# Performance work log

Measured on AMD Instinct MI355X. Metric: run time of the kernel, lower is better.

## Reference

```python
import jax, jax.numpy as jnp
import numpy as np

N, T, D, H = 256, 128, 512, 1024

def setup_inputs() -> dict:
    key = jax.random.key(0)
    k = jax.random.split(key, 5)
    x = jax.random.normal(k[0], (N, T, D), dtype=jnp.float32)
    A = jax.random.normal(k[1], (N, H, 4, 4), dtype=jnp.float32)
    Wx = jax.random.normal(k[2], (D, 4 * H), dtype=jnp.float32) / np.sqrt(D)
    Wh = jax.random.normal(k[3], (H, 4 * H), dtype=jnp.float32) / np.sqrt(H)
    Wattn = jax.random.normal(k[4], (H, 4 * H), dtype=jnp.float32) / np.sqrt(H)
    b = jnp.zeros((4 * H,), dtype=jnp.float32)
    return {"x": x, "A": A, "Wx": Wx, "Wh": Wh, "Wattn": Wattn, "b": b}

def reference(x, A, Wx, Wh, Wattn, b):
    n, h_dim = A.shape[0], A.shape[1]
    A_flat = A.reshape(n, h_dim, -1)            # (N, H, L), L = 16 spatial locations
    h0 = A_flat.mean(axis=-1)                   # avg-pooled image feature
    c0 = h0
    scale = 1.0 / jnp.sqrt(jnp.asarray(h_dim, dtype=x.dtype))

    def step(carry, x_t):
        h, c = carry
        # scaled dot-product attention over the 4x4 feature grid
        scores = jnp.einsum('nhl,nh->nl', A_flat, h) * scale
        w = jax.nn.softmax(scores, axis=1)
        attn = jnp.einsum('nhl,nl->nh', A_flat, w)
        gates = x_t @ Wx + h @ Wh + attn @ Wattn + b  # (N, 4H)
        i, f, o, g = jnp.split(gates, 4, axis=1)
        c_next = jax.nn.sigmoid(f) * c + jax.nn.sigmoid(i) * jnp.tanh(g)
        h_next = jax.nn.sigmoid(o) * jnp.tanh(c_next)
        return (h_next, c_next), h_next

    (_, _), hs = jax.lax.scan(step, (h0, c0), jnp.swapaxes(x, 0, 1))
    return jnp.swapaxes(hs, 0, 1)               # (N, T, H)
```

## Files before the change

kernel.cpp:

```cpp
#include <hip/hip_runtime.h>

#define Nn 256
#define Tt 128
#define Dd 512
#define Hh 1024
#define G4 4096
#define KK 2560
#define KSTEP 1536
#define KHALF 768

typedef __attribute__((ext_vector_type(8))) short s8v;
typedef __attribute__((ext_vector_type(4))) short s4v;
typedef __attribute__((ext_vector_type(4))) float f4v;

__device__ __forceinline__ float bf2f(ushort u) {
    union { unsigned int i; float f; } v; v.i = ((unsigned int)u) << 16; return v.f;
}
__device__ __forceinline__ ushort f2bf(float f) {
    union { float f; unsigned int i; } v; v.f = f;
    unsigned int x = v.i;
    return (ushort)((x + 0x7fffu + ((x >> 16) & 1u)) >> 16);
}
__device__ __forceinline__ void split2(float f, ushort& hi, ushort& lo) {
    hi = f2bf(f);
    lo = f2bf(f - bf2f(hi));
}

__global__ __launch_bounds__(256) void prep_W(
    const float* __restrict__ Wx, const float* __restrict__ Wh,
    const float* __restrict__ Wa, ushort* __restrict__ Whi,
    ushort* __restrict__ Wlo)
{
    __shared__ float tile[64 * 65];
    int kb = blockIdx.x * 64;
    int jb = blockIdx.y * 64;
    const float* src; int kofs;
    if (kb < Dd)            { src = Wx; kofs = kb; }
    else if (kb < Dd + Hh)  { src = Wh; kofs = kb - Dd; }
    else                    { src = Wa; kofs = kb - Dd - Hh; }
    int tid = threadIdx.x;
    int r = tid >> 2;
    int c16 = (tid & 3) * 16;
    const float* sp = src + (size_t)(kofs + r) * G4 + jb + c16;
    #pragma unroll
    for (int i = 0; i < 16; i++) tile[(c16 + i) * 65 + r] = sp[i];
    __syncthreads();
    ushort hi[16], lo[16];
    #pragma unroll
    for (int i = 0; i < 16; i++) split2(tile[r * 65 + c16 + i], hi[i], lo[i]);
    size_t o = (size_t)(jb + r) * KK + kb + c16;
    #pragma unroll
    for (int p = 0; p < 2; p++) {
        s8v vh, vl;
        #pragma unroll
        for (int i = 0; i < 8; i++) { vh[i] = (short)hi[p * 8 + i]; vl[i] = (short)lo[p * 8 + i]; }
        *(s8v*)&Whi[o + p * 8] = vh;
        *(s8v*)&Wlo[o + p * 8] = vl;
    }
}

__global__ __launch_bounds__(256) void prep_A(
    const float* __restrict__ A, ushort* __restrict__ Athi,
    ushort* __restrict__ Atlo)
{
    int n = blockIdx.x;
    int tid = threadIdx.x;
    int h0 = tid * 4;
    float v[4][16];
    #pragma unroll
    for (int r = 0; r < 4; r++) {
        const f4v* p = (const f4v*)(A + ((size_t)n * Hh + h0 + r) * 16);
        #pragma unroll
        for (int q = 0; q < 4; q++) {
            f4v xv = p[q];
            v[r][q * 4 + 0] = xv[0]; v[r][q * 4 + 1] = xv[1];
            v[r][q * 4 + 2] = xv[2]; v[r][q * 4 + 3] = xv[3];
        }
    }
    #pragma unroll
    for (int l = 0; l < 16; l++) {
        s4v vh, vl;
        #pragma unroll
        for (int r = 0; r < 4; r++) {
            ushort hi, lo; split2(v[r][l], hi, lo);
            vh[r] = (short)hi; vl[r] = (short)lo;
        }
        size_t o = ((size_t)n * 16 + l) * Hh + h0;
        *(s4v*)&Athi[o] = vh;
        *(s4v*)&Atlo[o] = vl;
    }
}

__global__ __launch_bounds__(256) void aw_gemm(
    const ushort* __restrict__ Athi, const ushort* __restrict__ Atlo,
    const ushort* __restrict__ Whi, const ushort* __restrict__ Wlo,
    float* __restrict__ AW)
{
    __shared__ ushort Ahi[64 * 72], Alo[64 * 72];
    __shared__ ushort Bhi[64 * 72], Blo[64 * 72];
    int j0 = blockIdx.x * 64;
    int m0 = blockIdx.y * 64;
    int tid = threadIdx.x;
    int lane = tid & 63, wave = tid >> 6;
    int l15 = lane & 15, quad = lane >> 4;
    f4v acc[4];
    #pragma unroll
    for (int s = 0; s < 4; s++) acc[s] = (f4v){0.f, 0.f, 0.f, 0.f};
    int rs = tid >> 3;
    int cs = (tid & 7) * 8;
    for (int kb = 0; kb < Hh; kb += 64) {
        __syncthreads();
        #pragma unroll
        for (int p = 0; p < 2; p++) {
            int r = rs + 32 * p;
            size_t oa = (size_t)(m0 + r) * Hh + kb + cs;
            *(s8v*)&Ahi[r * 72 + cs] = *(const s8v*)&Athi[oa];
            *(s8v*)&Alo[r * 72 + cs] = *(const s8v*)&Atlo[oa];
            size_t ob = (size_t)(j0 + r) * KK + (Dd + Hh) + kb + cs;
            *(s8v*)&Bhi[r * 72 + cs] = *(const s8v*)&Whi[ob];
            *(s8v*)&Blo[r * 72 + cs] = *(const s8v*)&Wlo[ob];
        }
        __syncthreads();
        #pragma unroll
        for (int ks = 0; ks < 2; ks++) {
            s8v ah = *(const s8v*)&Ahi[(wave * 16 + l15) * 72 + ks * 32 + quad * 8];
            s8v al = *(const s8v*)&Alo[(wave * 16 + l15) * 72 + ks * 32 + quad * 8];
            #pragma unroll
            for (int s = 0; s < 4; s++) {
                s8v bh = *(const s8v*)&Bhi[(s * 16 + l15) * 72 + ks * 32 + quad * 8];
                s8v bl = *(const s8v*)&Blo[(s * 16 + l15) * 72 + ks * 32 + quad * 8];
                acc[s] = __builtin_amdgcn_mfma_f32_16x16x32_bf16(ah, bh, acc[s], 0, 0, 0);
                acc[s] = __builtin_amdgcn_mfma_f32_16x16x32_bf16(ah, bl, acc[s], 0, 0, 0);
                acc[s] = __builtin_amdgcn_mfma_f32_16x16x32_bf16(al, bh, acc[s], 0, 0, 0);
            }
        }
    }
    #pragma unroll
    for (int s = 0; s < 4; s++) {
        int j = j0 + s * 16 + l15;
        #pragma unroll
        for (int rr = 0; rr < 4; rr++) {
            int row = m0 + wave * 16 + quad * 4 + rr;
            AW[(size_t)row * G4 + j] = acc[s][rr];
        }
    }
}

__global__ __launch_bounds__(256) void init_h0(
    const float* __restrict__ A, float* __restrict__ h, float* __restrict__ c,
    ushort* __restrict__ hhi, ushort* __restrict__ hlo)
{
    int i = blockIdx.x * 256 + threadIdx.x;
    const float* ap = A + (size_t)i * 16;
    float s = 0.f;
    #pragma unroll
    for (int l = 0; l < 16; l++) s += ap[l];
    s *= (1.f / 16.f);
    h[i] = s; c[i] = s;
    ushort hi, lo; split2(s, hi, lo);
    hhi[i] = hi; hlo[i] = lo;
}

__global__ __launch_bounds__(256) void calc_w(
    const float* __restrict__ A, const float* __restrict__ h,
    float* __restrict__ wbuf)
{
    int n = blockIdx.x;
    int tid = threadIdx.x;
    int lane = tid & 63, wave = tid >> 6;
    __shared__ float red[4][16];
    float part[16];
    #pragma unroll
    for (int l = 0; l < 16; l++) part[l] = 0.f;
    #pragma unroll
    for (int rr = 0; rr < 4; rr++) {
        int hh = tid + rr * 256;
        float hv = h[n * Hh + hh];
        const f4v* ap = (const f4v*)(A + ((size_t)n * Hh + hh) * 16);
        #pragma unroll
        for (int q = 0; q < 4; q++) {
            f4v v = ap[q];
            part[q * 4 + 0] += v[0] * hv; part[q * 4 + 1] += v[1] * hv;
            part[q * 4 + 2] += v[2] * hv; part[q * 4 + 3] += v[3] * hv;
        }
    }
    #pragma unroll
    for (int l = 0; l < 16; l++) {
        float v = part[l];
        #pragma unroll
        for (int off = 32; off > 0; off >>= 1) v += __shfl_down(v, off);
        if (lane == 0) red[wave][l] = v;
    }
    __syncthreads();
    if (tid == 0) {
        float sc[16]; float mx = -3.4e38f;
        #pragma unroll
        for (int l = 0; l < 16; l++) {
            sc[l] = (red[0][l] + red[1][l] + red[2][l] + red[3][l]) * 0.03125f;
            mx = fmaxf(mx, sc[l]);
        }
        float sum = 0.f;
        #pragma unroll
        for (int l = 0; l < 16; l++) { sc[l] = expf(sc[l] - mx); sum += sc[l]; }
        float inv = 1.f / sum;
        #pragma unroll
        for (int l = 0; l < 16; l++) wbuf[n * 16 + l] = sc[l] * inv;
    }
}

__global__ __launch_bounds__(256) void gemm_half(
    const float* __restrict__ x,
    const ushort* __restrict__ hhi, const ushort* __restrict__ hlo,
    const ushort* __restrict__ Whi, const ushort* __restrict__ Wlo,
    float* __restrict__ g0, float* __restrict__ g1, int t)
{
    __shared__ ushort Ahi[64 * 72], Alo[64 * 72];
    __shared__ ushort Bhi[64 * 72], Blo[64 * 72];
    int j0 = blockIdx.x * 64;
    int n0 = blockIdx.y * 64;
    int kb0 = blockIdx.z * KHALF;
    float* gout = blockIdx.z ? g1 : g0;
    int tid = threadIdx.x;
    int lane = tid & 63, wave = tid >> 6;
    int l15 = lane & 15, quad = lane >> 4;
    f4v acc[4];
    #pragma unroll
    for (int s = 0; s < 4; s++) acc[s] = (f4v){0.f, 0.f, 0.f, 0.f};

    int rs = tid >> 3;
    int cs = (tid & 7) * 8;

    for (int kb = kb0; kb < kb0 + KHALF; kb += 64) {
        __syncthreads();
        if (kb < Dd) {
            const float* xs = x + (size_t)t * Dd + kb + cs;
            #pragma unroll
            for (int p = 0; p < 2; p++) {
                int r = rs + 32 * p;
                const float* ap = xs + (size_t)(n0 + r) * (Tt * Dd);
                s8v vh, vl;
                #pragma unroll
                for (int i = 0; i < 8; i++) {
                    ushort hi_, lo_; split2(ap[i], hi_, lo_);
                    vh[i] = (short)hi_; vl[i] = (short)lo_;
                }
                *(s8v*)&Ahi[r * 72 + cs] = vh;
                *(s8v*)&Alo[r * 72 + cs] = vl;
            }
        } else {
            int kofs = kb - Dd;
            #pragma unroll
            for (int p = 0; p < 2; p++) {
                int r = rs + 32 * p;
                size_t o = (size_t)(n0 + r) * Hh + kofs + cs;
                *(s8v*)&Ahi[r * 72 + cs] = *(const s8v*)&hhi[o];
                *(s8v*)&Alo[r * 72 + cs] = *(const s8v*)&hlo[o];
            }
        }
        #pragma unroll
        for (int p = 0; p < 2; p++) {
            int r = rs + 32 * p;
            size_t o = (size_t)(j0 + r) * KK + kb + cs;
            *(s8v*)&Bhi[r * 72 + cs] = *(const s8v*)&Whi[o];
            *(s8v*)&Blo[r * 72 + cs] = *(const s8v*)&Wlo[o];
        }
        __syncthreads();
        #pragma unroll
        for (int ks = 0; ks < 2; ks++) {
            s8v ah = *(const s8v*)&Ahi[(wave * 16 + l15) * 72 + ks * 32 + quad * 8];
            s8v al = *(const s8v*)&Alo[(wave * 16 + l15) * 72 + ks * 32 + quad * 8];
            #pragma unroll
            for (int s = 0; s < 4; s++) {
                s8v bh = *(const s8v*)&Bhi[(s * 16 + l15) * 72 + ks * 32 + quad * 8];
                s8v bl = *(const s8v*)&Blo[(s * 16 + l15) * 72 + ks * 32 + quad * 8];
                acc[s] = __builtin_amdgcn_mfma_f32_16x16x32_bf16(ah, bh, acc[s], 0, 0, 0);
                acc[s] = __builtin_amdgcn_mfma_f32_16x16x32_bf16(ah, bl, acc[s], 0, 0, 0);
                acc[s] = __builtin_amdgcn_mfma_f32_16x16x32_bf16(al, bh, acc[s], 0, 0, 0);
            }
        }
    }
    #pragma unroll
    for (int s = 0; s < 4; s++) {
        int j = j0 + s * 16 + l15;
        #pragma unroll
        for (int rr = 0; rr < 4; rr++) {
            int row = n0 + wave * 16 + quad * 4 + rr;
            gout[(size_t)row * G4 + j] = acc[s][rr];
        }
    }
}

__global__ __launch_bounds__(256) void lstm_fused(
    const float* __restrict__ g0, const float* __restrict__ g1,
    const float* __restrict__ bias, const float* __restrict__ AW,
    float* __restrict__ wbuf, const float* __restrict__ A,
    float* __restrict__ c, ushort* __restrict__ hhi, ushort* __restrict__ hlo,
    float* __restrict__ out, int t)
{
    int n = blockIdx.x;
    int tid = threadIdx.x;
    int lane = tid & 63, wave = tid >> 6;
    int j4 = tid * 4;
    __shared__ float wsh[16];
    __shared__ float red[4][16];
    if (tid < 16) wsh[tid] = wbuf[n * 16 + tid];
    __syncthreads();
    float w[16];
    #pragma unroll
    for (int l = 0; l < 16; l++) w[l] = wsh[l];

    f4v acc[4];
    #pragma unroll
    for (int q = 0; q < 4; q++) acc[q] = (f4v){0.f, 0.f, 0.f, 0.f};
    const float* awp = AW + (size_t)n * 16 * G4;
    #pragma unroll
    for (int l = 0; l < 16; l++) {
        float wl = w[l];
        #pragma unroll
        for (int q = 0; q < 4; q++) {
            f4v v = *(const f4v*)&awp[(size_t)l * G4 + q * Hh + j4];
            acc[q][0] += wl * v[0]; acc[q][1] += wl * v[1];
            acc[q][2] += wl * v[2]; acc[q][3] += wl * v[3];
        }
    }

    size_t base = (size_t)n * G4;
    f4v gv[4];
    #pragma unroll
    for (int q = 0; q < 4; q++) {
        f4v a0 = *(const f4v*)&g0[base + q * Hh + j4];
        f4v a1 = *(const f4v*)&g1[base + q * Hh + j4];
        f4v bv = *(const f4v*)&bias[q * Hh + j4];
        #pragma unroll
        for (int e = 0; e < 4; e++) gv[q][e] = a0[e] + a1[e] + bv[e] + acc[q][e];
    }
    int i4 = n * Hh + j4;
    f4v cold = *(const f4v*)&c[i4];
    f4v cnew, hnew;
    #pragma unroll
    for (int e = 0; e < 4; e++) {
        float si = 1.f / (1.f + expf(-gv[0][e]));
        float sf = 1.f / (1.f + expf(-gv[1][e]));
        float so = 1.f / (1.f + expf(-gv[2][e]));
        float tg = tanhf(gv[3][e]);
        float cn = sf * cold[e] + si * tg;
        float hn = so * tanhf(cn);
        cnew[e] = cn; hnew[e] = hn;
    }
    *(f4v*)&c[i4] = cnew;
    s4v vh, vl;
    #pragma unroll
    for (int e = 0; e < 4; e++) {
        ushort hi, lo; split2(hnew[e], hi, lo);
        vh[e] = (short)hi; vl[e] = (short)lo;
    }
    *(s4v*)&hhi[i4] = vh;
    *(s4v*)&hlo[i4] = vl;
    *(f4v*)&out[((size_t)n * Tt + t) * Hh + j4] = hnew;

    float part[16];
    #pragma unroll
    for (int l = 0; l < 16; l++) part[l] = 0.f;
    #pragma unroll
    for (int r = 0; r < 4; r++) {
        float hv = hnew[r];
        const f4v* ap = (const f4v*)(A + ((size_t)n * Hh + j4 + r) * 16);
        #pragma unroll
        for (int q = 0; q < 4; q++) {
            f4v v = ap[q];
            part[q * 4 + 0] += v[0] * hv; part[q * 4 + 1] += v[1] * hv;
            part[q * 4 + 2] += v[2] * hv; part[q * 4 + 3] += v[3] * hv;
        }
    }
    #pragma unroll
    for (int l = 0; l < 16; l++) {
        float v = part[l];
        #pragma unroll
        for (int off = 32; off > 0; off >>= 1) v += __shfl_down(v, off);
        if (lane == 0) red[wave][l] = v;
    }
    __syncthreads();
    if (tid == 0) {
        float sc[16]; float mx = -3.4e38f;
        #pragma unroll
        for (int l = 0; l < 16; l++) {
            sc[l] = (red[0][l] + red[1][l] + red[2][l] + red[3][l]) * 0.03125f;
            mx = fmaxf(mx, sc[l]);
        }
        float sum = 0.f;
        #pragma unroll
        for (int l = 0; l < 16; l++) { sc[l] = expf(sc[l] - mx); sum += sc[l]; }
        float inv = 1.f / sum;
        #pragma unroll
        for (int l = 0; l < 16; l++) wbuf[n * 16 + l] = sc[l] * inv;
    }
}

extern "C" void kernel_launch(void* const* d_in, const int* in_sizes, int n_in,
                              void* d_out, int out_size, void* d_ws, size_t ws_size,
                              hipStream_t stream)
{
    const float* x  = (const float*)d_in[0];
    const float* A  = (const float*)d_in[1];
    const float* Wx = (const float*)d_in[2];
    const float* Wh = (const float*)d_in[3];
    const float* Wa = (const float*)d_in[4];
    const float* b  = (const float*)d_in[5];
    float* out = (float*)d_out;

    char* p = (char*)d_ws;
    ushort* Whi  = (ushort*)p;  p += (size_t)G4 * KK * 2;
    ushort* Wlo  = (ushort*)p;  p += (size_t)G4 * KK * 2;
    float*  h    = (float*)p;   p += (size_t)Nn * Hh * 4;
    float*  c    = (float*)p;   p += (size_t)Nn * Hh * 4;
    float*  g0   = (float*)p;   p += (size_t)Nn * G4 * 4;
    float*  g1   = (float*)p;   p += (size_t)Nn * G4 * 4;
    ushort* hhi  = (ushort*)p;  p += (size_t)Nn * Hh * 2;
    ushort* hlo  = (ushort*)p;  p += (size_t)Nn * Hh * 2;
    ushort* Athi = (ushort*)p;  p += (size_t)Nn * 16 * Hh * 2;
    ushort* Atlo = (ushort*)p;  p += (size_t)Nn * 16 * Hh * 2;
    float*  AW   = (float*)p;   p += (size_t)Nn * 16 * G4 * 4;
    float*  wbuf = (float*)p;   p += (size_t)Nn * 16 * 4;

    prep_W<<<dim3(KK / 64, G4 / 64), 256, 0, stream>>>(Wx, Wh, Wa, Whi, Wlo);
    prep_A<<<Nn, 256, 0, stream>>>(A, Athi, Atlo);
    aw_gemm<<<dim3(G4 / 64, (Nn * 16) / 64), 256, 0, stream>>>(
        Athi, Atlo, Whi, Wlo, AW);
    init_h0<<<(Nn * Hh) / 256, 256, 0, stream>>>(A, h, c, hhi, hlo);
    calc_w<<<Nn, 256, 0, stream>>>(A, h, wbuf);
    for (int t = 0; t < Tt; t++) {
        gemm_half<<<dim3(G4 / 64, Nn / 64, 2), 256, 0, stream>>>(
            x, hhi, hlo, Whi, Wlo, g0, g1, t);
        lstm_fused<<<Nn, 256, 0, stream>>>(
            g0, g1, b, AW, wbuf, A, c, hhi, hlo, out, t);
    }
}
```

Baseline: 5.936 ms.

## Double-buffer per-step GEMM with register prefetch and 128-row tiles

Rewrites the per-timestep gate GEMM to use two LDS buffers. The next K-slice of global data is loaded into registers while MFMAs run on the current slice, which leaves one barrier per iteration instead of two. The tile grows from 64 to 128 rows of N so each wave computes two 16-row subtiles, reusing B fragments and halving the number of weight loads per output. It also vectorizes the fp32 x loads. In exchange, the grid shrinks from 512 to 256 blocks, and LDS and register use rise, which limits occupancy (launch_bounds 256,1).

```diff
diff --git a/kernel.cpp b/kernel.cpp
--- a/kernel.cpp
+++ b/kernel.cpp
@@ -8,6 +8,7 @@
 #define KK 2560
 #define KSTEP 1536
 #define KHALF 768
+#define NIT 12
 
 typedef __attribute__((ext_vector_type(8))) short s8v;
 typedef __attribute__((ext_vector_type(4))) short s4v;
@@ -208,84 +209,126 @@
     }
 }
 
-__global__ __launch_bounds__(256) void gemm_half(
+__global__ __launch_bounds__(256, 1) void gemm_step(
     const float* __restrict__ x,
     const ushort* __restrict__ hhi, const ushort* __restrict__ hlo,
     const ushort* __restrict__ Whi, const ushort* __restrict__ Wlo,
     float* __restrict__ g0, float* __restrict__ g1, int t)
 {
-    __shared__ ushort Ahi[64 * 72], Alo[64 * 72];
-    __shared__ ushort Bhi[64 * 72], Blo[64 * 72];
-    int j0 = blockIdx.x * 64;
-    int n0 = blockIdx.y * 64;
-    int kb0 = blockIdx.z * KHALF;
+    __shared__ ushort Ah[2][128 * 72], Al[2][128 * 72];
+    __shared__ ushort Bh[2][64 * 72],  Bl[2][64 * 72];
+    const int j0 = blockIdx.x * 64;
+    const int n0 = blockIdx.y * 128;
+    const int kb0 = blockIdx.z * KHALF;
     float* gout = blockIdx.z ? g1 : g0;
-    int tid = threadIdx.x;
-    int lane = tid & 63, wave = tid >> 6;
-    int l15 = lane & 15, quad = lane >> 4;
-    f4v acc[4];
-    #pragma unroll
-    for (int s = 0; s < 4; s++) acc[s] = (f4v){0.f, 0.f, 0.f, 0.f};
-
-    int rs = tid >> 3;
-    int cs = (tid & 7) * 8;
-
-    for (int kb = kb0; kb < kb0 + KHALF; kb += 64) {
-        __syncthreads();
-        if (kb < Dd) {
-            const float* xs = x + (size_t)t * Dd + kb + cs;
-            #pragma unroll
-            for (int p = 0; p < 2; p++) {
-                int r = rs + 32 * p;
-                const float* ap = xs + (size_t)(n0 + r) * (Tt * Dd);
+    const int tid = threadIdx.x;
+    const int lane = tid & 63, wave = tid >> 6;
+    const int l15 = lane & 15, quad = lane >> 4;
+    const int rs = tid >> 3, cs = (tid & 7) * 8;
+
+    f4v acc[2][4];
+    #pragma unroll
+    for (int rt = 0; rt < 2; rt++)
+        #pragma unroll
+        for (int ct = 0; ct < 4; ct++) acc[rt][ct] = (f4v){0.f, 0.f, 0.f, 0.f};
+
+    f4v xr[4][2];
+    s8v arh[4], arl[4];
+    s8v brh[2], brl[2];
+    int ldx = 0;
+
+    auto LOADT = [&](int kb) {
+        ldx = (kb < Dd) ? 1 : 0;
+        if (ldx) {
+            #pragma unroll
+            for (int p = 0; p < 4; p++) {
+                const f4v* ap = (const f4v*)(x + ((size_t)(n0 + rs + 32 * p) * Tt + t) * Dd + kb + cs);
+                xr[p][0] = ap[0]; xr[p][1] = ap[1];
+            }
+        } else {
+            int ko = kb - Dd;
+            #pragma unroll
+            for (int p = 0; p < 4; p++) {
+                size_t o = (size_t)(n0 + rs + 32 * p) * Hh + ko + cs;
+                arh[p] = *(const s8v*)&hhi[o];
+                arl[p] = *(const s8v*)&hlo[o];
+            }
+        }
+        #pragma unroll
+        for (int p = 0; p < 2; p++) {
+            size_t o = (size_t)(j0 + rs + 32 * p) * KK + kb + cs;
+            brh[p] = *(const s8v*)&Whi[o];
+            brl[p] = *(const s8v*)&Wlo[o];
+        }
+    };
+    auto WRITET = [&](int b) {
+        if (ldx) {
+            #pragma unroll
+            for (int p = 0; p < 4; p++) {
                 s8v vh, vl;
                 #pragma unroll
-                for (int i = 0; i < 8; i++) {
-                    ushort hi_, lo_; split2(ap[i], hi_, lo_);
+                for (int i = 0; i < 4; i++) {
+                    ushort hi_, lo_;
+                    split2(xr[p][0][i], hi_, lo_);
                     vh[i] = (short)hi_; vl[i] = (short)lo_;
+                    split2(xr[p][1][i], hi_, lo_);
+                    vh[i + 4] = (short)hi_; vl[i + 4] = (short)lo_;
                 }
-                *(s8v*)&Ahi[r * 72 + cs] = vh;
-                *(s8v*)&Alo[r * 72 + cs] = vl;
+                *(s8v*)&Ah[b][(rs + 32 * p) * 72 + cs] = vh;
+                *(s8v*)&Al[b][(rs + 32 * p) * 72 + cs] = vl;
             }
         } else {
-            int kofs = kb - Dd;
-            #pragma unroll
-            for (int p = 0; p < 2; p++) {
-                int r = rs + 32 * p;
-                size_t o = (size_t)(n0 + r) * Hh + kofs + cs;
-                *(s8v*)&Ahi[r * 72 + cs] = *(const s8v*)&hhi[o];
-                *(s8v*)&Alo[r * 72 + cs] = *(const s8v*)&hlo[o];
+            #pragma unroll
+            for (int p = 0; p < 4; p++) {
+                *(s8v*)&Ah[b][(rs + 32 * p) * 72 + cs] = arh[p];
+                *(s8v*)&Al[b][(rs + 32 * p) * 72 + cs] = arl[p];
             }
         }
         #pragma unroll
         for (int p = 0; p < 2; p++) {
-            int r = rs + 32 * p;
-            size_t o = (size_t)(j0 + r) * KK + kb + cs;
-            *(s8v*)&Bhi[r * 72 + cs] = *(const s8v*)&Whi[o];
-            *(s8v*)&Blo[r * 72 + cs] = *(const s8v*)&Wlo[o];
-        }
+            *(s8v*)&Bh[b][(rs + 32 * p) * 72 + cs] = brh[p];
+            *(s8v*)&Bl[b][(rs + 32 * p) * 72 + cs] = brl[p];
+        }
+    };
+
+    LOADT(kb0);
+    WRITET(0);
+    __syncthreads();
+    int cur = 0;
+    for (int it = 0; it < NIT; it++) {
+        if (it + 1 < NIT) LOADT(kb0 + (it + 1) * 64);
+        #pragma unroll
+        for (int ks = 0; ks < 2; ks++) {
+            s8v ah0 = *(const s8v*)&Ah[cur][(wave * 32 + l15) * 72 + ks * 32 + quad * 8];
+            s8v ah1 = *(const s8v*)&Ah[cur][(wave * 32 + 16 + l15) * 72 + ks * 32 + quad * 8];
+            s8v al0 = *(const s8v*)&Al[cur][(wave * 32 + l15) * 72 + ks * 32 + quad * 8];
+            s8v al1 = *(const s8v*)&Al[cur][(wave * 32 + 16 + l15) * 72 + ks * 32 + quad * 8];
+            #pragma unroll
+            for (int ct = 0; ct < 4; ct++) {
+                s8v bh = *(const s8v*)&Bh[cur][(ct * 16 + l15) * 72 + ks * 32 + quad * 8];
+                s8v bl = *(const s8v*)&Bl[cur][(ct * 16 + l15) * 72 + ks * 32 + quad * 8];
+                acc[0][ct] = __builtin_amdgcn_mfma_f32_16x16x32_bf16(ah0, bh, acc[0][ct], 0, 0, 0);
+                acc[0][ct] = __builtin_amdgcn_mfma_f32_16x16x32_bf16(ah0, bl, acc[0][ct], 0, 0, 0);
+                acc[0][ct] = __builtin_amdgcn_mfma_f32_16x16x32_bf16(al0, bh, acc[0][ct], 0, 0, 0);
+                acc[1][ct] = __builtin_amdgcn_mfma_f32_16x16x32_bf16(ah1, bh, acc[1][ct], 0, 0, 0);
+                acc[1][ct] = __builtin_amdgcn_mfma_f32_16x16x32_bf16(ah1, bl, acc[1][ct], 0, 0, 0);
+                acc[1][ct] = __builtin_amdgcn_mfma_f32_16x16x32_bf16(al1, bh, acc[1][ct], 0, 0, 0);
+            }
+        }
+        if (it + 1 < NIT) WRITET(cur ^ 1);
         __syncthreads();
-        #pragma unroll
-        for (int ks = 0; ks < 2; ks++) {
-            s8v ah = *(const s8v*)&Ahi[(wave * 16 + l15) * 72 + ks * 32 + quad * 8];
-            s8v al = *(const s8v*)&Alo[(wave * 16 + l15) * 72 + ks * 32 + quad * 8];
-            #pragma unroll
-            for (int s = 0; s < 4; s++) {
-                s8v bh = *(const s8v*)&Bhi[(s * 16 + l15) * 72 + ks * 32 + quad * 8];
-                s8v bl = *(const s8v*)&Blo[(s * 16 + l15) * 72 + ks * 32 + quad * 8];
-                acc[s] = __builtin_amdgcn_mfma_f32_16x16x32_bf16(ah, bh, acc[s], 0, 0, 0);
-                acc[s] = __builtin_amdgcn_mfma_f32_16x16x32_bf16(ah, bl, acc[s], 0, 0, 0);
-                acc[s] = __builtin_amdgcn_mfma_f32_16x16x32_bf16(al, bh, acc[s], 0, 0, 0);
-            }
-        }
-    }
-    #pragma unroll
-    for (int s = 0; s < 4; s++) {
-        int j = j0 + s * 16 + l15;
-        #pragma unroll
-        for (int rr = 0; rr < 4; rr++) {
-            int row = n0 + wave * 16 + quad * 4 + rr;
-            gout[(size_t)row * G4 + j] = acc[s][rr];
+        cur ^= 1;
+    }
+    #pragma unroll
+    for (int rt = 0; rt < 2; rt++) {
+        #pragma unroll
+        for (int ct = 0; ct < 4; ct++) {
+            int j = j0 + ct * 16 + l15;
+            #pragma unroll
+            for (int rr = 0; rr < 4; rr++) {
+                int row = n0 + wave * 32 + rt * 16 + quad * 4 + rr;
+                gout[(size_t)row * G4 + j] = acc[rt][ct][rr];
+            }
         }
     }
 }
@@ -429,7 +472,7 @@
     init_h0<<<(Nn * Hh) / 256, 256, 0, stream>>>(A, h, c, hhi, hlo);
     calc_w<<<Nn, 256, 0, stream>>>(A, h, wbuf);
     for (int t = 0; t < Tt; t++) {
-        gemm_half<<<dim3(G4 / 64, Nn / 64, 2), 256, 0, stream>>>(
+        gemm_step<<<dim3(G4 / 64, Nn / 128, 2), 256, 0, stream>>>(
             x, hhi, hlo, Whi, Wlo, g0, g1, t);
         lstm_fused<<<Nn, 256, 0, stream>>>(
             g0, g1, b, AW, wbuf, A, c, hhi, hlo, out, t);
```

Result: no change. 6.023 ms (+1.5%).

## Use 128-row tiles with four-way split-K in step GEMM, store AW as fp16

Applied to the files above, without the earlier changes.

The per-step gate GEMM now uses 128x64 output tiles, with each wave computing two 16-row subtiles, and splits K into four 384-wide slices instead of two 768-wide ones. This keeps the grid at 512 blocks while reusing each loaded W tile across twice as many batch rows, which cuts W traffic per step. The precomputed attention projection AW is stored in fp16 instead of fp32, halving the bytes lstm_fused reads from it every step. In exchange, lstm_fused must read four partial-sum buffers instead of two, and the fp16 AW adds rounding error.

```diff
diff --git a/kernel.cpp b/kernel.cpp
--- a/kernel.cpp
+++ b/kernel.cpp
@@ -7,11 +7,14 @@
 #define G4 4096
 #define KK 2560
 #define KSTEP 1536
-#define KHALF 768
+#define KQ 384
+#define NIT 6
 
 typedef __attribute__((ext_vector_type(8))) short s8v;
 typedef __attribute__((ext_vector_type(4))) short s4v;
 typedef __attribute__((ext_vector_type(4))) float f4v;
+typedef _Float16 f16;
+typedef __attribute__((ext_vector_type(4))) _Float16 h4v;
 
 __device__ __forceinline__ float bf2f(ushort u) {
     union { unsigned int i; float f; } v; v.i = ((unsigned int)u) << 16; return v.f;
@@ -94,7 +97,7 @@
 __global__ __launch_bounds__(256) void aw_gemm(
     const ushort* __restrict__ Athi, const ushort* __restrict__ Atlo,
     const ushort* __restrict__ Whi, const ushort* __restrict__ Wlo,
-    float* __restrict__ AW)
+    f16* __restrict__ AW)
 {
     __shared__ ushort Ahi[64 * 72], Alo[64 * 72];
     __shared__ ushort Bhi[64 * 72], Blo[64 * 72];
@@ -141,7 +144,7 @@
         #pragma unroll
         for (int rr = 0; rr < 4; rr++) {
             int row = m0 + wave * 16 + quad * 4 + rr;
-            AW[(size_t)row * G4 + j] = acc[s][rr];
+            AW[(size_t)row * G4 + j] = (f16)acc[s][rr];
         }
     }
 }
@@ -208,34 +211,38 @@
     }
 }
 
-__global__ __launch_bounds__(256) void gemm_half(
+__global__ __launch_bounds__(256) void gemm_step(
     const float* __restrict__ x,
     const ushort* __restrict__ hhi, const ushort* __restrict__ hlo,
     const ushort* __restrict__ Whi, const ushort* __restrict__ Wlo,
-    float* __restrict__ g0, float* __restrict__ g1, int t)
-{
-    __shared__ ushort Ahi[64 * 72], Alo[64 * 72];
-    __shared__ ushort Bhi[64 * 72], Blo[64 * 72];
-    int j0 = blockIdx.x * 64;
-    int n0 = blockIdx.y * 64;
-    int kb0 = blockIdx.z * KHALF;
-    float* gout = blockIdx.z ? g1 : g0;
-    int tid = threadIdx.x;
-    int lane = tid & 63, wave = tid >> 6;
-    int l15 = lane & 15, quad = lane >> 4;
-    f4v acc[4];
-    #pragma unroll
-    for (int s = 0; s < 4; s++) acc[s] = (f4v){0.f, 0.f, 0.f, 0.f};
-
-    int rs = tid >> 3;
-    int cs = (tid & 7) * 8;
-
-    for (int kb = kb0; kb < kb0 + KHALF; kb += 64) {
+    float* __restrict__ g0, float* __restrict__ g1,
+    float* __restrict__ g2, float* __restrict__ g3, int t)
+{
+    __shared__ ushort Ah[128 * 72], Al[128 * 72];
+    __shared__ ushort Bh[64 * 72],  Bl[64 * 72];
+    const int j0 = blockIdx.x * 64;
+    const int n0 = blockIdx.y * 128;
+    const int kz = blockIdx.z;
+    const int kb0 = kz * KQ;
+    float* gout = (kz == 0) ? g0 : (kz == 1) ? g1 : (kz == 2) ? g2 : g3;
+    const int tid = threadIdx.x;
+    const int lane = tid & 63, wave = tid >> 6;
+    const int l15 = lane & 15, quad = lane >> 4;
+    const int rs = tid >> 3, cs = (tid & 7) * 8;
+
+    f4v acc[2][4];
+    #pragma unroll
+    for (int rt = 0; rt < 2; rt++)
+        #pragma unroll
+        for (int ct = 0; ct < 4; ct++) acc[rt][ct] = (f4v){0.f, 0.f, 0.f, 0.f};
+
+    for (int it = 0; it < NIT; it++) {
+        int kb = kb0 + it * 64;
         __syncthreads();
         if (kb < Dd) {
             const float* xs = x + (size_t)t * Dd + kb + cs;
             #pragma unroll
-            for (int p = 0; p < 2; p++) {
+            for (int p = 0; p < 4; p++) {
                 int r = rs + 32 * p;
                 const float* ap = xs + (size_t)(n0 + r) * (Tt * Dd);
                 s8v vh, vl;
@@ -244,55 +251,64 @@
                     ushort hi_, lo_; split2(ap[i], hi_, lo_);
                     vh[i] = (short)hi_; vl[i] = (short)lo_;
                 }
-                *(s8v*)&Ahi[r * 72 + cs] = vh;
-                *(s8v*)&Alo[r * 72 + cs] = vl;
+                *(s8v*)&Ah[r * 72 + cs] = vh;
+                *(s8v*)&Al[r * 72 + cs] = vl;
             }
         } else {
-            int kofs = kb - Dd;
+            int ko = kb - Dd;
             #pragma unroll
-            for (int p = 0; p < 2; p++) {
+            for (int p = 0; p < 4; p++) {
                 int r = rs + 32 * p;
-                size_t o = (size_t)(n0 + r) * Hh + kofs + cs;
-                *(s8v*)&Ahi[r * 72 + cs] = *(const s8v*)&hhi[o];
-                *(s8v*)&Alo[r * 72 + cs] = *(const s8v*)&hlo[o];
+                size_t o = (size_t)(n0 + r) * Hh + ko + cs;
+                *(s8v*)&Ah[r * 72 + cs] = *(const s8v*)&hhi[o];
+                *(s8v*)&Al[r * 72 + cs] = *(const s8v*)&hlo[o];
             }
         }
         #pragma unroll
         for (int p = 0; p < 2; p++) {
             int r = rs + 32 * p;
             size_t o = (size_t)(j0 + r) * KK + kb + cs;
-            *(s8v*)&Bhi[r * 72 + cs] = *(const s8v*)&Whi[o];
-            *(s8v*)&Blo[r * 72 + cs] = *(const s8v*)&Wlo[o];
+            *(s8v*)&Bh[r * 72 + cs] = *(const s8v*)&Whi[o];
+            *(s8v*)&Bl[r * 72 + cs] = *(const s8v*)&Wlo[o];
         }
         __syncthreads();
         #pragma unroll
         for (int ks = 0; ks < 2; ks++) {
-            s8v ah = *(const s8v*)&Ahi[(wave * 16 + l15) * 72 + ks * 32 + quad * 8];
-            s8v al = *(const s8v*)&Alo[(wave * 16 + l15) * 72 + ks * 32 + quad * 8];
+            s8v ah0 = *(const s8v*)&Ah[(wave * 32 + l15) * 72 + ks * 32 + quad * 8];
+            s8v ah1 = *(const s8v*)&Ah[(wave * 32 + 16 + l15) * 72 + ks * 32 + quad * 8];
+            s8v al0 = *(const s8v*)&Al[(wave * 32 + l15) * 72 + ks * 32 + quad * 8];
+            s8v al1 = *(const s8v*)&Al[(wave * 32 + 16 + l15) * 72 + ks * 32 + quad * 8];
             #pragma unroll
-            for (int s = 0; s < 4; s++) {
-                s8v bh = *(const s8v*)&Bhi[(s * 16 + l15) * 72 + ks * 32 + quad * 8];
-                s8v bl = *(const s8v*)&Blo[(s * 16 + l15) * 72 + ks * 32 + quad * 8];
-                acc[s] = __builtin_amdgcn_mfma_f32_16x16x32_bf16(ah, bh, acc[s], 0, 0, 0);
-                acc[s] = __builtin_amdgcn_mfma_f32_16x16x32_bf16(ah, bl, acc[s], 0, 0, 0);
-                acc[s] = __builtin_amdgcn_mfma_f32_16x16x32_bf16(al, bh, acc[s], 0, 0, 0);
+            for (int ct = 0; ct < 4; ct++) {
+                s8v bh = *(const s8v*)&Bh[(ct * 16 + l15) * 72 + ks * 32 + quad * 8];
+                s8v bl = *(const s8v*)&Bl[(ct * 16 + l15) * 72 + ks * 32 + quad * 8];
+                acc[0][ct] = __builtin_amdgcn_mfma_f32_16x16x32_bf16(ah0, bh, acc[0][ct], 0, 0, 0);
+                acc[0][ct] = __builtin_amdgcn_mfma_f32_16x16x32_bf16(ah0, bl, acc[0][ct], 0, 0, 0);
+                acc[0][ct] = __builtin_amdgcn_mfma_f32_16x16x32_bf16(al0, bh, acc[0][ct], 0, 0, 0);
+                acc[1][ct] = __builtin_amdgcn_mfma_f32_16x16x32_bf16(ah1, bh, acc[1][ct], 0, 0, 0);
+                acc[1][ct] = __builtin_amdgcn_mfma_f32_16x16x32_bf16(ah1, bl, acc[1][ct], 0, 0, 0);
+                acc[1][ct] = __builtin_amdgcn_mfma_f32_16x16x32_bf16(al1, bh, acc[1][ct], 0, 0, 0);
             }
         }
     }
     #pragma unroll
-    for (int s = 0; s < 4; s++) {
-        int j = j0 + s * 16 + l15;
-        #pragma unroll
-        for (int rr = 0; rr < 4; rr++) {
-            int row = n0 + wave * 16 + quad * 4 + rr;
-            gout[(size_t)row * G4 + j] = acc[s][rr];
+    for (int rt = 0; rt < 2; rt++) {
+        #pragma unroll
+        for (int ct = 0; ct < 4; ct++) {
+            int j = j0 + ct * 16 + l15;
+            #pragma unroll
+            for (int rr = 0; rr < 4; rr++) {
+                int row = n0 + wave * 32 + rt * 16 + quad * 4 + rr;
+                gout[(size_t)row * G4 + j] = acc[rt][ct][rr];
+            }
         }
     }
 }
 
 __global__ __launch_bounds__(256) void lstm_fused(
     const float* __restrict__ g0, const float* __restrict__ g1,
-    const float* __restrict__ bias, const float* __restrict__ AW,
+    const float* __restrict__ g2, const float* __restrict__ g3,
+    const float* __restrict__ bias, const f16* __restrict__ AW,
     float* __restrict__ wbuf, const float* __restrict__ A,
     float* __restrict__ c, ushort* __restrict__ hhi, ushort* __restrict__ hlo,
     float* __restrict__ out, int t)
@@ -312,15 +328,15 @@
     f4v acc[4];
     #pragma unroll
     for (int q = 0; q < 4; q++) acc[q] = (f4v){0.f, 0.f, 0.f, 0.f};
-    const float* awp = AW + (size_t)n * 16 * G4;
+    const f16* awp = AW + (size_t)n * 16 * G4;
     #pragma unroll
     for (int l = 0; l < 16; l++) {
         float wl = w[l];
         #pragma unroll
         for (int q = 0; q < 4; q++) {
-            f4v v = *(const f4v*)&awp[(size_t)l * G4 + q * Hh + j4];
-            acc[q][0] += wl * v[0]; acc[q][1] += wl * v[1];
-            acc[q][2] += wl * v[2]; acc[q][3] += wl * v[3];
+            h4v v = *(const h4v*)&awp[(size_t)l * G4 + q * Hh + j4];
+            acc[q][0] += wl * (float)v[0]; acc[q][1] += wl * (float)v[1];
+            acc[q][2] += wl * (float)v[2]; acc[q][3] += wl * (float)v[3];
         }
     }
 
@@ -330,9 +346,12 @@
     for (int q = 0; q < 4; q++) {
         f4v a0 = *(const f4v*)&g0[base + q * Hh + j4];
         f4v a1 = *(const f4v*)&g1[base + q * Hh + j4];
+        f4v a2 = *(const f4v*)&g2[base + q * Hh + j4];
+        f4v a3 = *(const f4v*)&g3[base + q * Hh + j4];
         f4v bv = *(const f4v*)&bias[q * Hh + j4];
         #pragma unroll
-        for (int e = 0; e < 4; e++) gv[q][e] = a0[e] + a1[e] + bv[e] + acc[q][e];
+        for (int e = 0; e < 4; e++)
+            gv[q][e] = (a0[e] + a1[e]) + (a2[e] + a3[e]) + bv[e] + acc[q][e];
     }
     int i4 = n * Hh + j4;
     f4v cold = *(const f4v*)&c[i4];
@@ -415,11 +434,13 @@
     float*  c    = (float*)p;   p += (size_t)Nn * Hh * 4;
     float*  g0   = (float*)p;   p += (size_t)Nn * G4 * 4;
     float*  g1   = (float*)p;   p += (size_t)Nn * G4 * 4;
+    float*  g2   = (float*)p;   p += (size_t)Nn * G4 * 4;
+    float*  g3   = (float*)p;   p += (size_t)Nn * G4 * 4;
     ushort* hhi  = (ushort*)p;  p += (size_t)Nn * Hh * 2;
     ushort* hlo  = (ushort*)p;  p += (size_t)Nn * Hh * 2;
     ushort* Athi = (ushort*)p;  p += (size_t)Nn * 16 * Hh * 2;
     ushort* Atlo = (ushort*)p;  p += (size_t)Nn * 16 * Hh * 2;
-    float*  AW   = (float*)p;   p += (size_t)Nn * 16 * G4 * 4;
+    f16*    AW   = (f16*)p;     p += (size_t)Nn * 16 * G4 * 2;
     float*  wbuf = (float*)p;   p += (size_t)Nn * 16 * 4;
 
     prep_W<<<dim3(KK / 64, G4 / 64), 256, 0, stream>>>(Wx, Wh, Wa, Whi, Wlo);
@@ -429,9 +450,9 @@
     init_h0<<<(Nn * Hh) / 256, 256, 0, stream>>>(A, h, c, hhi, hlo);
     calc_w<<<Nn, 256, 0, stream>>>(A, h, wbuf);
     for (int t = 0; t < Tt; t++) {
-        gemm_half<<<dim3(G4 / 64, Nn / 64, 2), 256, 0, stream>>>(
-            x, hhi, hlo, Whi, Wlo, g0, g1, t);
+        gemm_step<<<dim3(G4 / 64, Nn / 128, 4), 256, 0, stream>>>(
+            x, hhi, hlo, Whi, Wlo, g0, g1, g2, g3, t);
         lstm_fused<<<Nn, 256, 0, stream>>>(
-            g0, g1, b, AW, wbuf, A, c, hhi, hlo, out, t);
-    }
-}
+            g0, g1, g2, g3, b, AW, wbuf, A, c, hhi, hlo, out, t);
+    }
+}
```

New measurement: 5.196 ms. 1.14x faster.
